# Kernel optimization log

Measured on AMD Instinct MI355X. Metric: run time of the kernel, lower is better.

## Reference

```python
import jax, jax.numpy as jnp
import numpy as np

B, T = 128, 24
E = 512      # word_emb_size (== img feature dim)
H = 512      # hidden_size
V = 12000    # vocab_size


def setup_inputs() -> dict:
    key = jax.random.key(0)
    ks = jax.random.split(key, 8)
    s_e = 1.0 / np.sqrt(E)
    s_h = 1.0 / np.sqrt(H)
    return {
        "img": jax.random.normal(ks[0], (B, E), dtype=jnp.float32),
        "cap": jax.random.randint(ks[1], (B, T), 0, V, dtype=jnp.int64),
        "caplen": jax.random.randint(ks[2], (B,), 1, T + 1, dtype=jnp.int64),
        "emb": jax.random.normal(ks[3], (V, E), dtype=jnp.float32),
        "W_ih": jax.random.uniform(ks[4], (3 * H, E), jnp.float32, -s_h, s_h),
        "W_hh": jax.random.uniform(ks[5], (3 * H, H), jnp.float32, -s_h, s_h),
        "b_ih": jnp.zeros((3 * H,), jnp.float32),
        "b_hh": jnp.zeros((3 * H,), jnp.float32),
        "W_out": jax.random.uniform(ks[6], (V, H), jnp.float32, -s_h, s_h),
        "b_out": jax.random.uniform(ks[7], (V,), jnp.float32, -s_h, s_h),
    }


def _gru_decode(img, cap, emb, W_ih, W_hh, b_ih, b_hh, W_out, b_out):
    word_emb = emb[cap]                                   # [B, T, E]
    x_cat = jnp.concatenate([img[:, None, :], word_emb[:, :-1, :]], axis=1)  # [B, T, E]
    # Precompute input-gate projections for all steps (one big GEMM).
    gx = jnp.einsum('bte,ge->btg', x_cat, W_ih) + b_ih    # [B, T, 3H]
    h0 = jnp.zeros((img.shape[0], H), x_cat.dtype)

    def step(h, gx_t):
        gh = h @ W_hh.T + b_hh                            # [B, 3H]
        xr, xz, xn = jnp.split(gx_t, 3, axis=-1)
        hr, hz, hn = jnp.split(gh, 3, axis=-1)
        r = jax.nn.sigmoid(xr + hr)
        z = jax.nn.sigmoid(xz + hz)
        n = jnp.tanh(xn + r * hn)
        h_new = (1.0 - z) * n + z * h
        return h_new, h_new

    _, hs = jax.lax.scan(step, h0, jnp.swapaxes(gx, 0, 1))  # hs: [T, B, H]
    logits = jnp.einsum('tbh,vh->btv', hs, W_out) + b_out   # [B, T, V]
    return logits


def reference(img, cap, caplen, emb, W_ih, W_hh, b_ih, b_hh, W_out, b_out):
    # caplen only sets the (static here) unroll length in the original loop.
    predictions = _gru_decode(img, cap, emb, W_ih, W_hh, b_ih, b_hh, W_out, b_out)
    return predictions
```

## Files before the change

### kernel.cpp

```cpp
#include <hip/hip_runtime.h>
#include <hip/hip_bf16.h>
#include <cstdint>
#include <cstddef>

typedef __bf16 bf16;
typedef __bf16 bf16x8 __attribute__((ext_vector_type(8)));
typedef __bf16 bf16x4 __attribute__((ext_vector_type(4)));
typedef float  f32x4  __attribute__((ext_vector_type(4)));

#define TT 24
#define BB 128
#define EE 512
#define HH 512
#define VV 12000
#define VPAD 12032
#define THREEH 1536
#define MTOT (TT*BB)
#define NBLK 32

#define GLDS(gp, lp)                                                              \
  __builtin_amdgcn_global_load_lds(                                               \
      (const __attribute__((address_space(1))) void*)(const void*)(gp),           \
      (__attribute__((address_space(3))) void*)(void*)(lp), 16, 0, 0)
#define GLDS_COH(gp, lp)                                                          \
  __builtin_amdgcn_global_load_lds(                                               \
      (const __attribute__((address_space(1))) void*)(const void*)(gp),           \
      (__attribute__((address_space(3))) void*)(void*)(lp), 16, 0, 17)

#define QX   (MTOT*EE/4)
#define QIH  (THREEH*EE/4)
#define QHH  (THREEH*HH/4)
#define QOUT (VPAD*HH/4)
#define QTOT (QX+QIH+QHH+QOUT)

__global__ __launch_bounds__(256) void prep(const float* __restrict__ img,
                                            const int* __restrict__ cap,
                                            const float* __restrict__ emb,
                                            const float* __restrict__ W_ih,
                                            const float* __restrict__ W_hh,
                                            const float* __restrict__ W_out,
                                            bf16* __restrict__ X,
                                            bf16* __restrict__ Wih_b,
                                            bf16* __restrict__ Whh_b,
                                            bf16* __restrict__ Wout_b) {
  int q = blockIdx.x * 256 + threadIdx.x;
  if (q < QX) {
    int m = q >> 7, e4 = q & 127;
    int t = m >> 7, b = m & 127;
    const float* src;
    if (t == 0) src = img + (size_t)b * EE;
    else        src = emb + (size_t)cap[b * TT + (t - 1)] * EE;
    float4 v = *(const float4*)(src + e4 * 4);
    bf16x4 o = { (bf16)v.x, (bf16)v.y, (bf16)v.z, (bf16)v.w };
    *(bf16x4*)(X + (size_t)m * EE + e4 * 4) = o;
    return;
  }
  q -= QX;
  if (q < QIH) {
    float4 v = *(const float4*)(W_ih + (size_t)q * 4);
    bf16x4 o = { (bf16)v.x, (bf16)v.y, (bf16)v.z, (bf16)v.w };
    *(bf16x4*)(Wih_b + (size_t)q * 4) = o;
    return;
  }
  q -= QIH;
  if (q < QHH) {
    float4 v = *(const float4*)(W_hh + (size_t)q * 4);
    bf16x4 o = { (bf16)v.x, (bf16)v.y, (bf16)v.z, (bf16)v.w };
    *(bf16x4*)(Whh_b + (size_t)q * 4) = o;
    return;
  }
  q -= QHH;
  if (q < QOUT) {
    size_t i = (size_t)q * 4;
    float4 v = make_float4(0.f, 0.f, 0.f, 0.f);
    if (i + 4 <= (size_t)VV * HH) v = *(const float4*)(W_out + i);
    bf16x4 o = { (bf16)v.x, (bf16)v.y, (bf16)v.z, (bf16)v.w };
    *(bf16x4*)(Wout_b + i) = o;
  }
}

template <int PERM>
__global__ __launch_bounds__(256) void gemm_bt(const bf16* __restrict__ A,
                                               const bf16* __restrict__ Bm,
                                               const float* __restrict__ bias,
                                               float* __restrict__ C,
                                               int N, int Nvalid) {
  const int K = 512;
  __shared__ __align__(16) bf16 Alds[128 * 32];
  __shared__ __align__(16) bf16 Blds[128 * 32];
  const int tid  = threadIdx.x;
  const int lane = tid & 63;
  const int wv   = tid >> 6;
  const int wr   = wv >> 1, wc = wv & 1;

  const int nwg = gridDim.x * gridDim.y;
  const int wid = blockIdx.y * gridDim.x + blockIdx.x;
  const int cpx = nwg >> 3;
  const int swz = (wid & 7) * cpx + (wid >> 3);
  const int bx = swz % gridDim.x, by = swz / gridDim.x;

  const int m0 = by * 128, n0 = bx * 128;
  const bf16* Ab = A + (size_t)m0 * K;
  const bf16* Bb = Bm + (size_t)n0 * K;
  const int srow = tid >> 2;
  const int skq  = (tid & 3) * 8;

  f32x4 acc[4][4];
#pragma unroll
  for (int i = 0; i < 4; i++)
#pragma unroll
    for (int j = 0; j < 4; j++) acc[i][j] = 0.f;

  for (int kt = 0; kt < K; kt += 32) {
    __syncthreads();
    GLDS(Ab + (size_t)srow * K + kt + skq,        Alds + srow * 32 + skq);
    GLDS(Ab + (size_t)(srow + 64) * K + kt + skq, Alds + (srow + 64) * 32 + skq);
    GLDS(Bb + (size_t)srow * K + kt + skq,        Blds + srow * 32 + skq);
    GLDS(Bb + (size_t)(srow + 64) * K + kt + skq, Blds + (srow + 64) * 32 + skq);
    asm volatile("s_waitcnt vmcnt(0)" ::: "memory");
    __syncthreads();

    const int fr = lane & 15, kh = lane >> 4;
    bf16x8 af[4], bfv[4];
#pragma unroll
    for (int i = 0; i < 4; i++)
      af[i] = *(const bf16x8*)(Alds + (wr * 64 + i * 16 + fr) * 32 + kh * 8);
#pragma unroll
    for (int j = 0; j < 4; j++)
      bfv[j] = *(const bf16x8*)(Blds + (wc * 64 + j * 16 + fr) * 32 + kh * 8);
#pragma unroll
    for (int i = 0; i < 4; i++)
#pragma unroll
      for (int j = 0; j < 4; j++)
        acc[i][j] = __builtin_amdgcn_mfma_f32_16x16x32_bf16(af[i], bfv[j], acc[i][j], 0, 0, 0);
  }

  const int fr = lane & 15, fq = lane >> 4;
#pragma unroll
  for (int j = 0; j < 4; j++) {
    int n = n0 + wc * 64 + j * 16 + fr;
    if (n >= Nvalid) continue;
    float bv = bias ? bias[n] : 0.f;
#pragma unroll
    for (int i = 0; i < 4; i++) {
#pragma unroll
      for (int r = 0; r < 4; r++) {
        int m = m0 + wr * 64 + i * 16 + fq * 4 + r;
        float v = acc[i][j][r] + bv;
        size_t off;
        if (PERM) off = (size_t)(m & 127) * (TT * (size_t)VV) + (size_t)(m >> 7) * VV + n;
        else      off = (size_t)m * N + n;
        C[off] = v;
      }
    }
  }
}

__global__ __launch_bounds__(256) void gru_all(unsigned* __restrict__ HswA,
                                               unsigned* __restrict__ HswB,
                                               const bf16* __restrict__ Whh_b,
                                               const float* __restrict__ gx,
                                               const float* __restrict__ b_hh,
                                               bf16* __restrict__ hs,
                                               unsigned* __restrict__ flags) {
  __shared__ __align__(16) bf16 Wlds[48 * 512];
  __shared__ __align__(16) bf16 Alds[4][3][32 * 128];

  const int tid  = threadIdx.x;
  const int lane = tid & 63;
  const int wv   = tid >> 6;
  const int j0   = blockIdx.x * 16;
  const int fr   = lane & 15;
  const int kh   = lane >> 4;
  const int j    = j0 + fr;

#pragma unroll
  for (int i = 0; i < 12; ++i) {
    int r  = i * 4 + wv;
    int g  = r >> 4, jj = r & 15;
    bf16x8 v = *(const bf16x8*)(Whh_b + (size_t)(g * HH + j0 + jj) * 512 + lane * 8);
    int dst = r * 1024 + ((lane * 16) ^ ((r & 7) << 4));
    *(bf16x8*)((char*)Wlds + dst) = v;
  }
  __syncthreads();

  const float bh0 = b_hh[j], bh1 = b_hh[HH + j], bh2 = b_hh[2 * HH + j];

  float hreg[2][4];
#pragma unroll
  for (int mi = 0; mi < 2; mi++)
#pragma unroll
    for (int r = 0; r < 4; r++) hreg[mi][r] = 0.f;

  auto stageA = [&](const unsigned* hin, int kc, int buf) {
    const bf16* hb = (const bf16*)hin;
#pragma unroll
    for (int i = 0; i < 8; ++i) {
      int rr = i * 4 + kh;
      int cc = fr * 8;
      int src = (wv * 32 + rr) * 512 + kc * 128 + (cc ^ ((rr & 7) << 3));
      GLDS_COH(hb + src, &Alds[wv][buf][0] + rr * 128 + cc);
    }
  };

  f32x4 acc[2][3];
  auto computeKC = [&](int kc, int buf) {
#pragma unroll
    for (int kk = 0; kk < 4; ++kk) {
      bf16x8 af[2], bfv[3];
#pragma unroll
      for (int mi = 0; mi < 2; mi++)
        af[mi] = *(const bf16x8*)((char*)&Alds[wv][buf][0] +
                   (mi * 16 + fr) * 256 + ((kk * 64 + kh * 16) ^ ((fr & 7) << 4)));
#pragma unroll
      for (int g = 0; g < 3; g++)
        bfv[g] = *(const bf16x8*)((char*)Wlds + (g * 16 + fr) * 1024 +
                   ((kc * 256 + kk * 64 + kh * 16) ^ ((fr & 7) << 4)));
#pragma unroll
      for (int mi = 0; mi < 2; mi++)
#pragma unroll
        for (int g = 0; g < 3; g++)
          acc[mi][g] = __builtin_amdgcn_mfma_f32_16x16x32_bf16(af[mi], bfv[g], acc[mi][g], 0, 0, 0);
    }
  };

  float pxr[2][4], pxz[2][4], pxn[2][4];
  auto prefetchGX = [&](int t) {
#pragma unroll
    for (int mi = 0; mi < 2; mi++)
#pragma unroll
      for (int r = 0; r < 4; r++) {
        int bb = wv * 32 + mi * 16 + kh * 4 + r;
        const float* gb = gx + (size_t)(t * BB + bb) * THREEH + j;
        pxr[mi][r] = gb[0];
        pxz[mi][r] = gb[512];
        pxn[mi][r] = gb[1024];
      }
  };
  prefetchGX(0);

  for (int t = 0; t < TT; ++t) {
#pragma unroll
    for (int mi = 0; mi < 2; mi++)
#pragma unroll
      for (int g = 0; g < 3; g++) acc[mi][g] = 0.f;

    if (t > 0) {
      const unsigned* hi = (t & 1) ? HswA : HswB;
      stageA(hi, 0, 0);
      stageA(hi, 1, 1);
      stageA(hi, 2, 2);
      asm volatile("s_waitcnt vmcnt(16)" ::: "memory");
      computeKC(0, 0);
      asm volatile("s_waitcnt lgkmcnt(0)" ::: "memory");
      __builtin_amdgcn_sched_barrier(0);
      stageA(hi, 3, 0);
      asm volatile("s_waitcnt vmcnt(16)" ::: "memory");
      computeKC(1, 1);
      asm volatile("s_waitcnt vmcnt(8)" ::: "memory");
      computeKC(2, 2);
      asm volatile("s_waitcnt vmcnt(0)" ::: "memory");
      computeKC(3, 0);
    }

    unsigned* ho = (t & 1) ? HswB : HswA;
    unsigned* hs32 = (unsigned*)hs;
#pragma unroll
    for (int mi = 0; mi < 2; mi++) {
#pragma unroll
      for (int r = 0; r < 4; r++) {
        int bb  = wv * 32 + mi * 16 + kh * 4 + r;
        int row = t * BB + bb;
        float hr = acc[mi][0][r] + bh0;
        float hz = acc[mi][1][r] + bh1;
        float hn = acc[mi][2][r] + bh2;
        float rg = 1.f / (1.f + __expf(-(pxr[mi][r] + hr)));
        float zg = 1.f / (1.f + __expf(-(pxz[mi][r] + hz)));
        float ng = tanhf(pxn[mi][r] + rg * hn);
        float hnew = (1.f - zg) * ng + zg * hreg[mi][r];
        hreg[mi][r] = hnew;
        unsigned mine  = (unsigned)__builtin_bit_cast(unsigned short, (bf16)hnew);
        unsigned other = (unsigned)__shfl_xor((int)mine, 1);
        if (!(lane & 1)) {
          unsigned word = mine | (other << 16);
          int elem = bb * 512 + j;
          __hip_atomic_store(&ho[elem >> 1], word, __ATOMIC_RELAXED, __HIP_MEMORY_SCOPE_AGENT);
          hs32[((size_t)row * 512 + j) >> 1] = word;
        }
      }
    }

    if (t < TT - 1) {
      __syncthreads();
      if (tid == 0)
        __hip_atomic_store(&flags[(t * NBLK + blockIdx.x) * 4], 1u,
                           __ATOMIC_RELAXED, __HIP_MEMORY_SCOPE_AGENT);
      prefetchGX(t + 1);
      if (wv == 0 && lane < NBLK) {
        while (__hip_atomic_load(&flags[(t * NBLK + lane) * 4],
                                 __ATOMIC_RELAXED, __HIP_MEMORY_SCOPE_AGENT) == 0)
          __builtin_amdgcn_s_sleep(1);
      }
      __syncthreads();
    }
  }
}

extern "C" void kernel_launch(void* const* d_in, const int* in_sizes, int n_in,
                              void* d_out, int out_size, void* d_ws, size_t ws_size,
                              hipStream_t stream) {
  const float* img   = (const float*)d_in[0];
  const int*   cap   = (const int*)d_in[1];
  const float* emb   = (const float*)d_in[3];
  const float* W_ih  = (const float*)d_in[4];
  const float* W_hh  = (const float*)d_in[5];
  const float* b_ih  = (const float*)d_in[6];
  const float* b_hh  = (const float*)d_in[7];
  const float* W_out = (const float*)d_in[8];
  const float* b_out = (const float*)d_in[9];
  float* out = (float*)d_out;

  char* ws = (char*)d_ws;
  size_t off = 0;
  auto alloc = [&](size_t bytes) {
    void* p = ws + off;
    off = (off + bytes + 255) & ~(size_t)255;
    return p;
  };
  bf16*  X      = (bf16*)alloc((size_t)MTOT * EE * 2);
  bf16*  Wih_b  = (bf16*)alloc((size_t)THREEH * EE * 2);
  bf16*  Whh_b  = (bf16*)alloc((size_t)THREEH * HH * 2);
  bf16*  Wout_b = (bf16*)alloc((size_t)VPAD * HH * 2);
  float* gx     = (float*)alloc((size_t)MTOT * THREEH * 4);
  bf16*  hs     = (bf16*)alloc((size_t)MTOT * HH * 2);
  unsigned* HswA = (unsigned*)alloc((size_t)BB * HH * 2);
  unsigned* HswB = (unsigned*)alloc((size_t)BB * HH * 2);
  unsigned* flags = (unsigned*)alloc((size_t)TT * NBLK * 16);

  hipMemsetAsync(flags, 0, (size_t)TT * NBLK * 16, stream);

  prep<<<dim3((QTOT + 255) / 256), dim3(256), 0, stream>>>(
      img, cap, emb, W_ih, W_hh, W_out, X, Wih_b, Whh_b, Wout_b);

  gemm_bt<0><<<dim3(THREEH / 128, MTOT / 128), dim3(256), 0, stream>>>(
      X, Wih_b, b_ih, gx, THREEH, THREEH);

  gru_all<<<dim3(NBLK), dim3(256), 0, stream>>>(HswA, HswB, Whh_b, gx, b_hh, hs, flags);

  gemm_bt<1><<<dim3(VPAD / 128, MTOT / 128), dim3(256), 0, stream>>>(
      hs, Wout_b, b_out, out, VV, VV);
}
```

Before: 425.4 us.

## Double-buffer GEMM LDS with XOR swizzle and use raw coherent flag polling

The bf16 GEMM now double-buffers its LDS tiles, prefetching the next K slice with global_load_lds while MFMAs run on the current one. It applies an XOR swizzle on the K offset to cut LDS bank conflicts, and drops the workgroup-ID remap in favour of plain block indices. In the recurrent GRU kernel, the inter-block flag store and spin-poll become inline asm global store/load with sc0 sc1 cache bits and no s_sleep, aiming to shorten barrier latency. The risks are higher LDS use per block, the loss of the L2-locality swizzle, and heavier polling traffic.

```diff
diff --git a/kernel.cpp b/kernel.cpp
--- a/kernel.cpp
+++ b/kernel.cpp
@@ -86,24 +86,18 @@
                                                float* __restrict__ C,
                                                int N, int Nvalid) {
   const int K = 512;
-  __shared__ __align__(16) bf16 Alds[128 * 32];
-  __shared__ __align__(16) bf16 Blds[128 * 32];
+  __shared__ __align__(16) bf16 Alds[2][128 * 32];
+  __shared__ __align__(16) bf16 Blds[2][128 * 32];
   const int tid  = threadIdx.x;
   const int lane = tid & 63;
   const int wv   = tid >> 6;
   const int wr   = wv >> 1, wc = wv & 1;
-
-  const int nwg = gridDim.x * gridDim.y;
-  const int wid = blockIdx.y * gridDim.x + blockIdx.x;
-  const int cpx = nwg >> 3;
-  const int swz = (wid & 7) * cpx + (wid >> 3);
-  const int bx = swz % gridDim.x, by = swz / gridDim.x;
-
-  const int m0 = by * 128, n0 = bx * 128;
+  const int m0 = blockIdx.y * 128, n0 = blockIdx.x * 128;
   const bf16* Ab = A + (size_t)m0 * K;
   const bf16* Bb = Bm + (size_t)n0 * K;
   const int srow = tid >> 2;
   const int skq  = (tid & 3) * 8;
+  const int sksw = skq ^ ((srow & 3) * 8);
 
   f32x4 acc[4][4];
 #pragma unroll
@@ -111,31 +105,48 @@
 #pragma unroll
     for (int j = 0; j < 4; j++) acc[i][j] = 0.f;
 
-  for (int kt = 0; kt < K; kt += 32) {
-    __syncthreads();
-    GLDS(Ab + (size_t)srow * K + kt + skq,        Alds + srow * 32 + skq);
-    GLDS(Ab + (size_t)(srow + 64) * K + kt + skq, Alds + (srow + 64) * 32 + skq);
-    GLDS(Bb + (size_t)srow * K + kt + skq,        Blds + srow * 32 + skq);
-    GLDS(Bb + (size_t)(srow + 64) * K + kt + skq, Blds + (srow + 64) * 32 + skq);
-    asm volatile("s_waitcnt vmcnt(0)" ::: "memory");
-    __syncthreads();
-
-    const int fr = lane & 15, kh = lane >> 4;
+  auto stage = [&](int kt, int buf) {
+    GLDS(Ab + (size_t)srow * K + kt + sksw,        Alds[buf] + srow * 32 + skq);
+    GLDS(Ab + (size_t)(srow + 64) * K + kt + sksw, Alds[buf] + (srow + 64) * 32 + skq);
+    GLDS(Bb + (size_t)srow * K + kt + sksw,        Blds[buf] + srow * 32 + skq);
+    GLDS(Bb + (size_t)(srow + 64) * K + kt + sksw, Blds[buf] + (srow + 64) * 32 + skq);
+  };
+
+  stage(0, 0);
+  asm volatile("s_waitcnt vmcnt(0)" ::: "memory");
+  __syncthreads();
+
+  const int fr = lane & 15, kh = lane >> 4;
+  for (int it = 0; it < 16; ++it) {
+    const int buf = it & 1;
+    if (it < 15) stage((it + 1) * 32, buf ^ 1);
+
     bf16x8 af[4], bfv[4];
 #pragma unroll
-    for (int i = 0; i < 4; i++)
-      af[i] = *(const bf16x8*)(Alds + (wr * 64 + i * 16 + fr) * 32 + kh * 8);
-#pragma unroll
-    for (int j = 0; j < 4; j++)
-      bfv[j] = *(const bf16x8*)(Blds + (wc * 64 + j * 16 + fr) * 32 + kh * 8);
+    for (int i = 0; i < 4; i++) {
+      int row = wr * 64 + i * 16 + fr;
+      af[i] = *(const bf16x8*)((const char*)(Alds[buf] + row * 32) +
+                               ((kh * 16) ^ ((row & 3) << 4)));
+    }
+#pragma unroll
+    for (int j = 0; j < 4; j++) {
+      int row = wc * 64 + j * 16 + fr;
+      bfv[j] = *(const bf16x8*)((const char*)(Blds[buf] + row * 32) +
+                                ((kh * 16) ^ ((row & 3) << 4)));
+    }
 #pragma unroll
     for (int i = 0; i < 4; i++)
 #pragma unroll
       for (int j = 0; j < 4; j++)
         acc[i][j] = __builtin_amdgcn_mfma_f32_16x16x32_bf16(af[i], bfv[j], acc[i][j], 0, 0, 0);
-  }
-
-  const int fr = lane & 15, fq = lane >> 4;
+
+    if (it < 15) {
+      asm volatile("s_waitcnt vmcnt(0)" ::: "memory");
+      __syncthreads();
+    }
+  }
+
+  const int fq = lane >> 4;
 #pragma unroll
   for (int j = 0; j < 4; j++) {
     int n = n0 + wc * 64 + j * 16 + fr;
@@ -292,14 +303,20 @@
 
     if (t < TT - 1) {
       __syncthreads();
-      if (tid == 0)
-        __hip_atomic_store(&flags[(t * NBLK + blockIdx.x) * 4], 1u,
-                           __ATOMIC_RELAXED, __HIP_MEMORY_SCOPE_AGENT);
+      if (tid == 0) {
+        unsigned* fsp = &flags[(t * NBLK + blockIdx.x) * 4];
+        asm volatile("global_store_dword %0, %1, off sc0 sc1\n\t"
+                     "s_waitcnt vmcnt(0)" :: "v"(fsp), "v"(1u) : "memory");
+      }
       prefetchGX(t + 1);
       if (wv == 0 && lane < NBLK) {
-        while (__hip_atomic_load(&flags[(t * NBLK + lane) * 4],
-                                 __ATOMIC_RELAXED, __HIP_MEMORY_SCOPE_AGENT) == 0)
-          __builtin_amdgcn_s_sleep(1);
+        const unsigned* fpp = &flags[(t * NBLK + lane) * 4];
+        unsigned fv;
+        do {
+          asm volatile("global_load_dword %0, %1, off sc0 sc1\n\t"
+                       "s_waitcnt vmcnt(0)"
+                       : "=v"(fv) : "v"(fpp) : "memory");
+        } while (fv == 0);
       }
       __syncthreads();
     }
```

Result: no change. 432.3 us (+1.6%).
